# Optimization experiments

Hardware: AMD Instinct MI355X
Metric: run time of the kernel (lower is better)

## Reference

```python
import jax, jax.numpy as jnp
from jax import lax
import numpy as np

H = 256   # hidden size (hard-coded in module)
V = 10    # output classes


def setup_inputs() -> dict:
    key = jax.random.key(0)
    ks = jax.random.split(key, 7)
    B, T = 2048, 256
    x = jax.random.normal(ks[0], (B, T, 1), dtype=jnp.float32)
    # Linear weights stored as (in, out); torch nn.Linear computes x @ W.T + b,
    # equivalent here to x @ W_inout + b.
    s1 = 1.0  # fan_in of embed is 1
    sH = 1.0 / np.sqrt(H)
    W_e = jax.random.uniform(ks[1], (1, H), jnp.float32, -s1, s1)
    b_e = jax.random.uniform(ks[2], (H,), jnp.float32, -s1, s1)
    W_h = jax.random.uniform(ks[3], (H, H), jnp.float32, -sH, sH)
    b_h = jax.random.uniform(ks[4], (H,), jnp.float32, -sH, sH)
    W_o = jax.random.uniform(ks[5], (H, V), jnp.float32, -sH, sH)
    b_o = jax.random.uniform(ks[6], (V,), jnp.float32, -sH, sH)
    return {"x": x, "W_e": W_e, "b_e": b_e, "W_h": W_h, "b_h": b_h,
            "W_o": W_o, "b_o": b_o}


def reference(x, W_e, b_e, W_h, b_h, W_o, b_o):
    B, T, _ = x.shape
    # Embedding of each timestep is independent of h -> precompute in one batched op.
    inp_all = jnp.tanh(x @ W_e + b_e)            # [B, T, H]
    inp_tbh = jnp.swapaxes(inp_all, 0, 1)        # [T, B, H] for scan

    def step(h, inp_t):
        h = jnp.tanh((inp_t + h) @ W_h + b_h)    # [B, H]
        return h, None

    h0 = jnp.zeros((B, H), dtype=x.dtype)
    h_final, _ = lax.scan(step, h0, inp_tbh)
    return h_final @ W_o + b_o                   # [B, V]
```

## Files before the change

### kernel.cpp

```cpp
#include <hip/hip_runtime.h>

#define HDIM 256
#define TDIM 256
#define VOUT 10
#define BC   8

typedef _Float16 f16x8 __attribute__((ext_vector_type(8)));
typedef _Float16 f16x2 __attribute__((ext_vector_type(2)));
typedef float    f32x4 __attribute__((ext_vector_type(4)));

__device__ __forceinline__ float fast_tanh(float a) {
    float e = __expf(2.0f * a);
    return 1.0f - 2.0f * __builtin_amdgcn_rcpf(e + 1.0f);
}

__global__ __launch_bounds__(512, 2) void rnn_fwd_v6(
    const float* __restrict__ x,
    const float* __restrict__ We,
    const float* __restrict__ be,
    const float* __restrict__ Wh,
    const float* __restrict__ bh,
    const float* __restrict__ Wo,
    const float* __restrict__ bo,
    float* __restrict__ out)
{
    __shared__ __align__(16) char  vraw[2][BC * HDIM * 2];
    __shared__ __align__(16) float inp_lds[4][BC * HDIM];
    __shared__ float x_lds[BC][TDIM + 2];
    __shared__ float h_fin[BC][HDIM + 1];

    const int tid = threadIdx.x;
    const int l   = tid & 63;
    const int w   = tid >> 6;
    const int n   = l & 15;
    const int rn  = n & 7;
    const int hi  = n >> 3;
    const int g   = l >> 4;
    const int r0  = blockIdx.x * BC;

    for (int k = tid; k < BC * TDIM; k += 512) {
        int r = k >> 8, t = k & 255;
        x_lds[r][t] = x[(r0 + r) * TDIM + t];
    }

    f16x8 wfrag[2][8];
    #pragma unroll
    for (int mt = 0; mt < 2; ++mt) {
        const int col = 32 * w + 16 * mt + n;
        #pragma unroll
        for (int kt = 0; kt < 8; ++kt) {
            #pragma unroll
            for (int e = 0; e < 8; ++e)
                wfrag[mt][kt][e] = (_Float16)Wh[(kt * 32 + g * 8 + e) * HDIM + col];
        }
    }

    float bhf[2][4];
    #pragma unroll
    for (int mt = 0; mt < 2; ++mt)
        #pragma unroll
        for (int rg = 0; rg < 4; ++rg)
            bhf[mt][rg] = bh[32 * w + 16 * mt + 4 * g + rg];

    const int c_b  = tid >> 4;
    const int rn_b = (tid >> 1) & 7;
    const int hf_b = tid & 1;
    float Web[4], beb[4];
    #pragma unroll
    for (int r = 0; r < 4; ++r) {
        Web[r] = We[c_b * 8 + hf_b * 4 + r];
        beb[r] = be[c_b * 8 + hf_b * 4 + r];
    }
    const int bidx = c_b * 64 + rn_b * 8 + hf_b * 4;

    const int base_r = g * 128 + rn * 16;
    int addr_w[2];
    #pragma unroll
    for (int mt = 0; mt < 2; ++mt)
        addr_w[mt] = (4 * w + 2 * mt + (g >> 1)) * 128 + rn * 16 + (g & 1) * 8 + hi * 4;
    int iidx[2];
    #pragma unroll
    for (int mt = 0; mt < 2; ++mt)
        iidx[mt] = (4 * w + 2 * mt + (g >> 1)) * 64 + rn * 8 + (g & 1) * 4 + hi * 2;

    __syncthreads();

    #pragma unroll
    for (int tq = 0; tq < 3; ++tq) {
        const float xv = x_lds[rn_b][tq];
        f32x4 pk;
        #pragma unroll
        for (int r = 0; r < 4; ++r)
            pk[r] = fast_tanh(xv * Web[r] + beb[r]);
        *(f32x4*)&inp_lds[tq][bidx] = pk;
    }
    __syncthreads();

    #pragma unroll
    for (int mt = 0; mt < 2; ++mt) {
        const float v0 = inp_lds[0][iidx[mt] + 0];
        const float v1 = inp_lds[0][iidx[mt] + 1];
        f16x2 pk; pk[0] = (_Float16)v0; pk[1] = (_Float16)v1;
        *(f16x2*)(&vraw[0][0] + addr_w[mt]) = pk;
    }
    __syncthreads();

    int cur = 0;
    #pragma unroll 1
    for (int t = 0; t < TDIM; ++t) {
        const char* vr = &vraw[cur][0];
        const bool last = (t + 1 == TDIM);

        f16x8 bfrag[8];
        #pragma unroll
        for (int kt = 0; kt < 8; ++kt)
            bfrag[kt] = *(const f16x8*)(vr + base_r + kt * 512);

        float ip[2][2];
        {
            const float* ipl = &inp_lds[(t + 1) & 3][0];
            #pragma unroll
            for (int mt = 0; mt < 2; ++mt) {
                ip[mt][0] = ipl[iidx[mt] + 0];
                ip[mt][1] = ipl[iidx[mt] + 1];
            }
        }

        {
            const int tq = t + 3;
            if (tq < TDIM) {
                const float xv = x_lds[rn_b][tq];
                f32x4 pk;
                #pragma unroll
                for (int r = 0; r < 4; ++r)
                    pk[r] = fast_tanh(xv * Web[r] + beb[r]);
                *(f32x4*)&inp_lds[tq & 3][bidx] = pk;
            }
        }

        f32x4 accE[2], accO[2];
        #pragma unroll
        for (int mt = 0; mt < 2; ++mt) {
            accE[mt][0] = bhf[mt][0]; accE[mt][1] = bhf[mt][1];
            accE[mt][2] = bhf[mt][2]; accE[mt][3] = bhf[mt][3];
            accO[mt][0] = 0.0f; accO[mt][1] = 0.0f;
            accO[mt][2] = 0.0f; accO[mt][3] = 0.0f;
        }
        #pragma unroll
        for (int kp = 0; kp < 4; ++kp) {
            #pragma unroll
            for (int mt = 0; mt < 2; ++mt)
                accE[mt] = __builtin_amdgcn_mfma_f32_16x16x32_f16(
                    wfrag[mt][2 * kp], bfrag[2 * kp], accE[mt], 0, 0, 0);
            #pragma unroll
            for (int mt = 0; mt < 2; ++mt)
                accO[mt] = __builtin_amdgcn_mfma_f32_16x16x32_f16(
                    wfrag[mt][2 * kp + 1], bfrag[2 * kp + 1], accO[mt], 0, 0, 0);
        }

        if (!last) {
            char* vw = &vraw[cur ^ 1][0];
            #pragma unroll
            for (int mt = 0; mt < 2; ++mt) {
                const float a0 = hi ? (accE[mt][2] + accO[mt][2]) : (accE[mt][0] + accO[mt][0]);
                const float a1 = hi ? (accE[mt][3] + accO[mt][3]) : (accE[mt][1] + accO[mt][1]);
                const float s0 = fast_tanh(a0) + ip[mt][0];
                const float s1 = fast_tanh(a1) + ip[mt][1];
                f16x2 pk; pk[0] = (_Float16)s0; pk[1] = (_Float16)s1;
                *(f16x2*)(vw + addr_w[mt]) = pk;
            }
        } else {
            #pragma unroll
            for (int mt = 0; mt < 2; ++mt) {
                const float a0 = hi ? (accE[mt][2] + accO[mt][2]) : (accE[mt][0] + accO[mt][0]);
                const float a1 = hi ? (accE[mt][3] + accO[mt][3]) : (accE[mt][1] + accO[mt][1]);
                const int hc = 32 * w + 16 * mt + 4 * g + 2 * hi;
                h_fin[rn][hc + 0] = fast_tanh(a0);
                h_fin[rn][hc + 1] = fast_tanh(a1);
            }
        }
        cur ^= 1;
        __syncthreads();
    }

    if (tid < BC * VOUT) {
        const int r = tid / VOUT, vc = tid - r * VOUT;
        float sacc = bo[vc];
        #pragma unroll 8
        for (int i = 0; i < HDIM; ++i)
            sacc = fmaf(h_fin[r][i], Wo[i * VOUT + vc], sacc);
        out[(r0 + r) * VOUT + vc] = sacc;
    }
}

extern "C" void kernel_launch(void* const* d_in, const int* in_sizes, int n_in,
                              void* d_out, int out_size, void* d_ws, size_t ws_size,
                              hipStream_t stream) {
    const float* x  = (const float*)d_in[0];
    const float* We = (const float*)d_in[1];
    const float* be = (const float*)d_in[2];
    const float* Wh = (const float*)d_in[3];
    const float* bh = (const float*)d_in[4];
    const float* Wo = (const float*)d_in[5];
    const float* bo = (const float*)d_in[6];
    float* out = (float*)d_out;

    const int B = in_sizes[0] / TDIM;
    const int nblocks = B / BC;

    rnn_fwd_v6<<<nblocks, 512, 0, stream>>>(x, We, be, Wh, bh, Wo, bo, out);
}
```

Measured before the change: 178.9 us.

## Halve batch rows per block and use four waves each owning 64 hidden columns

```diff
diff --git a/kernel.cpp b/kernel.cpp
--- a/kernel.cpp
+++ b/kernel.cpp
@@ -3,10 +3,9 @@
 #define HDIM 256
 #define TDIM 256
 #define VOUT 10
-#define BC   8
+#define BC   4
 
 typedef _Float16 f16x8 __attribute__((ext_vector_type(8)));
-typedef _Float16 f16x2 __attribute__((ext_vector_type(2)));
 typedef float    f32x4 __attribute__((ext_vector_type(4)));
 
 __device__ __forceinline__ float fast_tanh(float a) {
@@ -14,7 +13,15 @@
     return 1.0f - 2.0f * __builtin_amdgcn_rcpf(e + 1.0f);
 }
 
-__global__ __launch_bounds__(512, 2) void rnn_fwd_v6(
+__device__ __forceinline__ float sel4(f32x4 v, int al) {
+    float r = v[0];
+    r = (al == 1) ? v[1] : r;
+    r = (al == 2) ? v[2] : r;
+    r = (al == 3) ? v[3] : r;
+    return r;
+}
+
+__global__ __launch_bounds__(256, 2) void rnn_fwd_v7(
     const float* __restrict__ x,
     const float* __restrict__ We,
     const float* __restrict__ be,
@@ -33,20 +40,22 @@
     const int l   = tid & 63;
     const int w   = tid >> 6;
     const int n   = l & 15;
-    const int rn  = n & 7;
-    const int hi  = n >> 3;
+    const int rn  = n & 3;
+    const int al  = n >> 2;
     const int g   = l >> 4;
+    const int u   = 4 * g + al;
+    const int o   = u & 7;
     const int r0  = blockIdx.x * BC;
 
-    for (int k = tid; k < BC * TDIM; k += 512) {
+    for (int k = tid; k < BC * TDIM; k += 256) {
         int r = k >> 8, t = k & 255;
         x_lds[r][t] = x[(r0 + r) * TDIM + t];
     }
 
-    f16x8 wfrag[2][8];
-    #pragma unroll
-    for (int mt = 0; mt < 2; ++mt) {
-        const int col = 32 * w + 16 * mt + n;
+    f16x8 wfrag[4][8];
+    #pragma unroll
+    for (int mt = 0; mt < 4; ++mt) {
+        const int col = 64 * w + 16 * mt + n;
         #pragma unroll
         for (int kt = 0; kt < 8; ++kt) {
             #pragma unroll
@@ -55,15 +64,15 @@
         }
     }
 
-    float bhf[2][4];
-    #pragma unroll
-    for (int mt = 0; mt < 2; ++mt)
+    float bhf[4][4];
+    #pragma unroll
+    for (int mt = 0; mt < 4; ++mt)
         #pragma unroll
         for (int rg = 0; rg < 4; ++rg)
-            bhf[mt][rg] = bh[32 * w + 16 * mt + 4 * g + rg];
-
-    const int c_b  = tid >> 4;
-    const int rn_b = (tid >> 1) & 7;
+            bhf[mt][rg] = bh[64 * w + 16 * mt + 4 * g + rg];
+
+    const int c_b  = tid >> 3;
+    const int rn_b = (tid >> 1) & 3;
     const int hf_b = tid & 1;
     float Web[4], beb[4];
     #pragma unroll
@@ -71,17 +80,16 @@
         Web[r] = We[c_b * 8 + hf_b * 4 + r];
         beb[r] = be[c_b * 8 + hf_b * 4 + r];
     }
-    const int bidx = c_b * 64 + rn_b * 8 + hf_b * 4;
-
-    const int base_r = g * 128 + rn * 16;
-    int addr_w[2];
-    #pragma unroll
-    for (int mt = 0; mt < 2; ++mt)
-        addr_w[mt] = (4 * w + 2 * mt + (g >> 1)) * 128 + rn * 16 + (g & 1) * 8 + hi * 4;
-    int iidx[2];
-    #pragma unroll
-    for (int mt = 0; mt < 2; ++mt)
-        iidx[mt] = (4 * w + 2 * mt + (g >> 1)) * 64 + rn * 8 + (g & 1) * 4 + hi * 2;
+    const int bidx = c_b * 32 + rn_b * 8 + hf_b * 4;
+
+    int addr_w[4], iidx[4];
+    #pragma unroll
+    for (int mt = 0; mt < 4; ++mt) {
+        const int c = 8 * w + 2 * mt + (u >> 3);
+        addr_w[mt] = c * 64 + rn * 16 + o * 2;
+        iidx[mt]   = c * 32 + rn * 8 + o;
+    }
+    const int base_r = g * 64 + rn * 16;
 
     __syncthreads();
 
@@ -97,12 +105,8 @@
     __syncthreads();
 
     #pragma unroll
-    for (int mt = 0; mt < 2; ++mt) {
-        const float v0 = inp_lds[0][iidx[mt] + 0];
-        const float v1 = inp_lds[0][iidx[mt] + 1];
-        f16x2 pk; pk[0] = (_Float16)v0; pk[1] = (_Float16)v1;
-        *(f16x2*)(&vraw[0][0] + addr_w[mt]) = pk;
-    }
+    for (int mt = 0; mt < 4; ++mt)
+        *(_Float16*)(&vraw[0][0] + addr_w[mt]) = (_Float16)inp_lds[0][iidx[mt]];
     __syncthreads();
 
     int cur = 0;
@@ -114,16 +118,14 @@
         f16x8 bfrag[8];
         #pragma unroll
         for (int kt = 0; kt < 8; ++kt)
-            bfrag[kt] = *(const f16x8*)(vr + base_r + kt * 512);
-
-        float ip[2][2];
+            bfrag[kt] = *(const f16x8*)(vr + base_r + kt * 256);
+
+        float ip[4];
         {
             const float* ipl = &inp_lds[(t + 1) & 3][0];
             #pragma unroll
-            for (int mt = 0; mt < 2; ++mt) {
-                ip[mt][0] = ipl[iidx[mt] + 0];
-                ip[mt][1] = ipl[iidx[mt] + 1];
-            }
+            for (int mt = 0; mt < 4; ++mt)
+                ip[mt] = ipl[iidx[mt]];
         }
 
         {
@@ -138,9 +140,9 @@
             }
         }
 
-        f32x4 accE[2], accO[2];
-        #pragma unroll
-        for (int mt = 0; mt < 2; ++mt) {
+        f32x4 accE[4], accO[4];
+        #pragma unroll
+        for (int mt = 0; mt < 4; ++mt) {
             accE[mt][0] = bhf[mt][0]; accE[mt][1] = bhf[mt][1];
             accE[mt][2] = bhf[mt][2]; accE[mt][3] = bhf[mt][3];
             accO[mt][0] = 0.0f; accO[mt][1] = 0.0f;
@@ -149,11 +151,11 @@
         #pragma unroll
         for (int kp = 0; kp < 4; ++kp) {
             #pragma unroll
-            for (int mt = 0; mt < 2; ++mt)
+            for (int mt = 0; mt < 4; ++mt)
                 accE[mt] = __builtin_amdgcn_mfma_f32_16x16x32_f16(
                     wfrag[mt][2 * kp], bfrag[2 * kp], accE[mt], 0, 0, 0);
             #pragma unroll
-            for (int mt = 0; mt < 2; ++mt)
+            for (int mt = 0; mt < 4; ++mt)
                 accO[mt] = __builtin_amdgcn_mfma_f32_16x16x32_f16(
                     wfrag[mt][2 * kp + 1], bfrag[2 * kp + 1], accO[mt], 0, 0, 0);
         }
@@ -161,22 +163,16 @@
         if (!last) {
             char* vw = &vraw[cur ^ 1][0];
             #pragma unroll
-            for (int mt = 0; mt < 2; ++mt) {
-                const float a0 = hi ? (accE[mt][2] + accO[mt][2]) : (accE[mt][0] + accO[mt][0]);
-                const float a1 = hi ? (accE[mt][3] + accO[mt][3]) : (accE[mt][1] + accO[mt][1]);
-                const float s0 = fast_tanh(a0) + ip[mt][0];
-                const float s1 = fast_tanh(a1) + ip[mt][1];
-                f16x2 pk; pk[0] = (_Float16)s0; pk[1] = (_Float16)s1;
-                *(f16x2*)(vw + addr_w[mt]) = pk;
+            for (int mt = 0; mt < 4; ++mt) {
+                const float a = sel4(accE[mt], al) + sel4(accO[mt], al);
+                const float s = fast_tanh(a) + ip[mt];
+                *(_Float16*)(vw + addr_w[mt]) = (_Float16)s;
             }
         } else {
             #pragma unroll
-            for (int mt = 0; mt < 2; ++mt) {
-                const float a0 = hi ? (accE[mt][2] + accO[mt][2]) : (accE[mt][0] + accO[mt][0]);
-                const float a1 = hi ? (accE[mt][3] + accO[mt][3]) : (accE[mt][1] + accO[mt][1]);
-                const int hc = 32 * w + 16 * mt + 4 * g + 2 * hi;
-                h_fin[rn][hc + 0] = fast_tanh(a0);
-                h_fin[rn][hc + 1] = fast_tanh(a1);
+            for (int mt = 0; mt < 4; ++mt) {
+                const float a = sel4(accE[mt], al) + sel4(accO[mt], al);
+                h_fin[rn][64 * w + 16 * mt + 4 * g + al] = fast_tanh(a);
             }
         }
         cur ^= 1;
@@ -208,5 +204,5 @@
     const int B = in_sizes[0] / TDIM;
     const int nblocks = B / BC;
 
-    rnn_fwd_v6<<<nblocks, 512, 0, stream>>>(x, We, be, Wh, bh, Wo, bo, out);
-}
+    rnn_fwd_v7<<<nblocks, 256, 0, stream>>>(x, We, be, Wh, bh, Wo, bo, out);
+}
```

Result: slower. 263.4 us (+47.2%).
